# Kernel tuning notes

Hardware: AMD Instinct MI355X
Metric: run time of the kernel (lower is better)

The kernel has to match this reference:

```python
import jax, jax.numpy as jnp
import numpy as np

NLT_SIZES = (10, 19, 39, 69, 12)  # agent, action, duplex, triplet, loc
ALPHA, GAMMA, BETA = 0.25, 2.0, 1.0 / 9.0
B, A, G, T = 8, 60000, 20, 5
C = 1 + sum(NLT_SIZES)  # 150


def setup_inputs() -> dict:
    key = jax.random.key(0)
    ks = jax.random.split(key, 8)
    confidence = jax.random.normal(ks[0], (B, A, C), jnp.float32)
    predicted_locations = jax.random.normal(ks[1], (B, A, 4), jnp.float32)
    gt_locations = jax.random.normal(ks[2], (B, A, 4), jnp.float32)
    counts = jax.random.randint(ks[3], (B,), 1, G + 1, dtype=jnp.int32)
    # gt_labels: [B, G, nlts, T] with -1 tail padding per (gt, label-type) row
    labs = []
    for i, nc in enumerate(NLT_SIZES):
        l = jax.random.randint(jax.random.fold_in(ks[4], i), (B, G, T), 0, nc, dtype=jnp.int32)
        nvalid = jax.random.randint(jax.random.fold_in(ks[5], i), (B, G, 1), 1, T + 1, dtype=jnp.int32)
        l = jnp.where(jnp.arange(T, dtype=jnp.int32)[None, None, :] < nvalid, l, -1)
        labs.append(l)
    gt_labels = jnp.stack(labs, axis=2)  # [B, G, 5, T]
    # labels_bin: per-anchor match result: -1 ignore, 0 background, k in [1, counts[b]] matched gt
    pos_idx = jax.random.randint(ks[6], (B, A), 1, G + 1, dtype=jnp.int32)
    pos_idx = jnp.minimum(pos_idx, counts[:, None])
    u = jax.random.uniform(ks[7], (B, A))
    labels_bin = jnp.where(u < 0.90, 0, jnp.where(u < 0.95, -1, pos_idx)).astype(jnp.int32)
    return {
        "confidence": confidence,
        "predicted_locations": predicted_locations,
        "gt_locations": gt_locations,
        "gt_labels": gt_labels,
        "counts": counts,
        "labels_bin": labels_bin,
    }


def _head_labels(gt_labels_nlt, labels_bin, numc):
    # gt_labels_nlt: [B, G, T] int, -1 tail-padded. Vectorized one_hot_labels + gather.
    valid = (gt_labels_nlt >= 0)
    oh = jax.nn.one_hot(jnp.where(valid, gt_labels_nlt, 0), numc, dtype=jnp.float32)
    oh = oh * valid[..., None].astype(jnp.float32)
    table = (oh.sum(axis=2) > 0).astype(jnp.float32)  # [B, G, numc], multi-hot per gt
    table = jnp.pad(table, ((0, 0), (1, 0), (0, 0)))  # row 0 = background zeros -> [B, G+1, numc]
    idx = jnp.clip(labels_bin, 0, None)  # dumy_conf: ignores (-1) map to row 0
    return jnp.take_along_axis(table, idx[:, :, None], axis=1)  # [B, A, numc]


def _focal(preds, labels, mask, num_pos):
    p = jnp.clip(preds, 1e-7, 1.0 - 1e-7)
    bce = -(labels * jnp.log(p) + (1.0 - labels) * jnp.log1p(-p))
    alpha_factor = ALPHA * labels + (1.0 - ALPHA) * (1.0 - labels)
    pt = p * labels + (1.0 - p) * (1.0 - labels)
    return (bce * alpha_factor * (1.0 - pt) ** GAMMA * mask).sum() / num_pos


def reference(confidence, predicted_locations, gt_locations, gt_labels, counts, labels_bin):
    sig = jax.nn.sigmoid(confidence)
    binary_preds = sig[:, :, 0]
    heads = []
    cc = 1
    for nc in NLT_SIZES:
        heads.append(sig[:, :, cc:cc + nc])
        cc += nc

    pos = (labels_bin > 0).astype(jnp.float32)  # pos_mask
    num_pos = jnp.maximum(1.0, pos.sum())

    n = jnp.abs(predicted_locations - gt_locations)
    sl1 = jnp.where(n < BETA, 0.5 * n * n / BETA, n - 0.5 * BETA)
    regression_loss = (sl1 * pos[:, :, None]).sum() / (num_pos * 4.0)

    mask = (labels_bin > -1).astype(jnp.float32)  # exclude ignored anchors
    cls_loss = 0.0
    for i, nc in enumerate(NLT_SIZES):
        labs = _head_labels(gt_labels[:, :, i, :], labels_bin, nc)
        cls_loss = cls_loss + _focal(heads[i], labs, mask[:, :, None], num_pos)
    cls_loss = cls_loss + _focal(binary_preds, pos, mask, num_pos)  # binary head: labels_bin>0 -> 1
    return (regression_loss, cls_loss / 6.0)
```

## Files before the change

### kernel.cpp

```cpp
#include <hip/hip_runtime.h>

#define B_     8
#define A_     60000
#define C_     150
#define G_     20
#define T_     5
#define ROWS   21
#define NANCH  (B_ * A_)
#define NTOT   (B_ * A_ * C_)
#define NCHUNK (NTOT / 4)
#define TABN   (B_ * ROWS * C_)
#define BETA_  (1.0f / 9.0f)
#define NBLK   8192
#define TPB    256

__global__ void build_table(const int* __restrict__ gt_labels,
                            float* __restrict__ tab) {
    int i = blockIdx.x * blockDim.x + threadIdx.x;
    if (i >= TABN) return;
    int c  = i % C_;
    int bg = i / C_;
    int g  = bg % ROWS;
    int b  = bg / ROWS;
    float v = 0.0f;
    if (g > 0) {
        if (c == 0) {
            v = 1.0f;
        } else {
            int cc = c - 1;
            int head, k;
            if      (cc < 10)  { head = 0; k = cc; }
            else if (cc < 29)  { head = 1; k = cc - 10; }
            else if (cc < 68)  { head = 2; k = cc - 29; }
            else if (cc < 137) { head = 3; k = cc - 68; }
            else               { head = 4; k = cc - 137; }
            const int* lp = gt_labels + ((b * G_ + (g - 1)) * 5 + head) * T_;
            v = (lp[0] == k || lp[1] == k || lp[2] == k ||
                 lp[3] == k || lp[4] == k) ? 1.0f : 0.0f;
        }
    }
    tab[i] = v;
}

__device__ __forceinline__ float block_reduce_sum(float v, float* sm) {
    #pragma unroll
    for (int off = 32; off > 0; off >>= 1) v += __shfl_down(v, off, 64);
    int lane = threadIdx.x & 63, w = threadIdx.x >> 6;
    if (lane == 0) sm[w] = v;
    __syncthreads();
    float r = 0.0f;
    if (threadIdx.x == 0) r = sm[0] + sm[1] + sm[2] + sm[3];
    __syncthreads();
    return r;
}

__device__ __forceinline__ float sl1(float n) {
    return (n < BETA_) ? (0.5f / BETA_) * n * n : n - 0.5f * BETA_;
}

__device__ __forceinline__ float focal_term(float x, float L, float mf) {
    float s     = (L + L - 1.0f) * x;
    float t     = __expf(-s);
    float denom = 1.0f + t;
    float om    = t * __builtin_amdgcn_rcpf(denom);
    float ld    = __logf(denom);
    return mf * fmaf(L, -0.5f, 0.75f) * (om * om) * ld;
}

__device__ __forceinline__ float process_chunk(float4 x, int a, int c,
                                               int l0, int l1,
                                               const float* __restrict__ tab) {
    float acc = 0.0f;
    float xs[4] = {x.x, x.y, x.z, x.w};
    if (!__any((l0 | l1) != 0)) {
        #pragma unroll
        for (int j = 0; j < 4; ++j) {
            float t     = __expf(xs[j]);
            float denom = 1.0f + t;
            float om    = t * __builtin_amdgcn_rcpf(denom);
            acc += 0.75f * (om * om) * __logf(denom);
        }
    } else {
        int   b0   = a / A_;
        int   row0 = (b0 * ROWS + max(l0, 0)) * C_;
        float m0   = (l0 > -1) ? 1.0f : 0.0f;
        int   row1 = row0;
        float m1   = m0;
        if (c + 3 >= C_) {
            int b1 = (a + 1) / A_;
            row1 = (b1 * ROWS + max(l1, 0)) * C_;
            m1   = (l1 > -1) ? 1.0f : 0.0f;
        }
        #pragma unroll
        for (int j = 0; j < 4; ++j) {
            int cj = c + j;
            int rb; float mf;
            if (cj < C_) { rb = row0 + cj;       mf = m0; }
            else         { rb = row1 + cj - C_;  mf = m1; }
            acc += focal_term(xs[j], tab[rb], mf);
        }
    }
    return acc;
}

__global__ __launch_bounds__(TPB) void fused_kernel(
        const float* __restrict__ conf,
        const float* __restrict__ pred, const float* __restrict__ gtl,
        const int*   __restrict__ lb,   const float* __restrict__ tab,
        float* __restrict__ partials) {
    __shared__ float sm[4];
    float reg = 0.0f, cls = 0.0f, cnt = 0.0f;
    const int tid    = blockIdx.x * blockDim.x + threadIdx.x;
    const int stride = gridDim.x * blockDim.x;

    for (int a = tid; a < NANCH; a += stride) {
        int l = lb[a];
        if (l > 0) {
            cnt += 1.0f;
            float4 p = ((const float4*)pred)[a];
            float4 g = ((const float4*)gtl)[a];
            reg += sl1(fabsf(p.x - g.x)) + sl1(fabsf(p.y - g.y)) +
                   sl1(fabsf(p.z - g.z)) + sl1(fabsf(p.w - g.w));
        }
    }

    const float4* cp = (const float4*)conf;
    int ch = tid;
    for (; ch + stride < NCHUNK; ch += 2 * stride) {
        const int chA = ch, chB = ch + stride;
        float4 xA = cp[chA];
        float4 xB = cp[chB];
        int eA = chA * 4, aA = eA / C_, cA = eA - aA * C_;
        int eB = chB * 4, aB = eB / C_, cB = eB - aB * C_;
        int lA0 = lb[aA];
        int lA1 = (cA + 3 >= C_) ? lb[aA + 1] : lA0;
        int lB0 = lb[aB];
        int lB1 = (cB + 3 >= C_) ? lb[aB + 1] : lB0;
        cls += process_chunk(xA, aA, cA, lA0, lA1, tab);
        cls += process_chunk(xB, aB, cB, lB0, lB1, tab);
    }
    if (ch < NCHUNK) {
        float4 x = cp[ch];
        int e = ch * 4, a = e / C_, c = e - a * C_;
        int l0 = lb[a];
        int l1 = (c + 3 >= C_) ? lb[a + 1] : l0;
        cls += process_chunk(x, a, c, l0, l1, tab);
    }

    float rb = block_reduce_sum(reg, sm);
    float cb = block_reduce_sum(cls, sm);
    float nb = block_reduce_sum(cnt, sm);
    if (threadIdx.x == 0) {
        float4 w; w.x = rb; w.y = cb; w.z = nb; w.w = 0.0f;
        ((float4*)partials)[blockIdx.x] = w;
    }
}

__global__ __launch_bounds__(TPB) void finalize(
        const float* __restrict__ partials, float* __restrict__ out) {
    __shared__ float sm[4];
    float r = 0.0f, c = 0.0f, n = 0.0f;
    for (int i = threadIdx.x; i < NBLK; i += TPB) {
        float4 p = ((const float4*)partials)[i];
        r += p.x; c += p.y; n += p.z;
    }
    r = block_reduce_sum(r, sm);
    c = block_reduce_sum(c, sm);
    n = block_reduce_sum(n, sm);
    if (threadIdx.x == 0) {
        float np = fmaxf(1.0f, n);
        out[0] = r / (np * 4.0f);
        out[1] = c / (np * 6.0f);
    }
}

extern "C" void kernel_launch(void* const* d_in, const int* in_sizes, int n_in,
                              void* d_out, int out_size, void* d_ws, size_t ws_size,
                              hipStream_t stream) {
    const float* conf = (const float*)d_in[0];
    const float* pred = (const float*)d_in[1];
    const float* gt   = (const float*)d_in[2];
    const int*   gtl  = (const int*)d_in[3];
    const int*   lb   = (const int*)d_in[5];
    float* out      = (float*)d_out;
    float* partials = (float*)d_ws;
    float* tab      = (float*)d_ws + 4 * NBLK;

    build_table<<<(TABN + TPB - 1) / TPB, TPB, 0, stream>>>(gtl, tab);
    fused_kernel<<<NBLK, TPB, 0, stream>>>(conf, pred, gt, lb, tab, partials);
    finalize<<<1, TPB, 0, stream>>>(partials, out);
}
```

Baseline: 408.6 us.

## Assign wave-sized tiles of confidence chunks and use wave-uniform label loads

The confidence loop now hands each wavefront a contiguous 256-element tile instead of striding chunks per thread. Each tile spans at most three anchors, so the labels are loaded once per wave as uniform scalar loads, and the all-background fast path becomes a uniform branch rather than a ballot. The loop is unrolled by four tiles with nontemporal loads to raise memory-level parallelism and avoid polluting the cache. The finalize kernel is also widened to 1024 threads. The costs are extra index math for tiles that cross anchor or batch boundaries, and more live registers from the deeper unroll.

Measured after the change: 403.7 us. About the same (-1.2%).

```diff
diff --git a/kernel.cpp b/kernel.cpp
--- a/kernel.cpp
+++ b/kernel.cpp
@@ -9,10 +9,14 @@
 #define NANCH  (B_ * A_)
 #define NTOT   (B_ * A_ * C_)
 #define NCHUNK (NTOT / 4)
+#define NTILE  (NCHUNK / 64)
 #define TABN   (B_ * ROWS * C_)
 #define BETA_  (1.0f / 9.0f)
 #define NBLK   8192
 #define TPB    256
+#define FTPB   1024
+
+typedef float f4 __attribute__((ext_vector_type(4)));
 
 __global__ void build_table(const int* __restrict__ gt_labels,
                             float* __restrict__ tab) {
@@ -42,6 +46,7 @@
     tab[i] = v;
 }
 
+template <int NW>
 __device__ __forceinline__ float block_reduce_sum(float v, float* sm) {
     #pragma unroll
     for (int off = 32; off > 0; off >>= 1) v += __shfl_down(v, off, 64);
@@ -49,7 +54,10 @@
     if (lane == 0) sm[w] = v;
     __syncthreads();
     float r = 0.0f;
-    if (threadIdx.x == 0) r = sm[0] + sm[1] + sm[2] + sm[3];
+    if (threadIdx.x == 0) {
+        #pragma unroll
+        for (int i = 0; i < NW; ++i) r += sm[i];
+    }
     __syncthreads();
     return r;
 }
@@ -67,37 +75,45 @@
     return mf * fmaf(L, -0.5f, 0.75f) * (om * om) * ld;
 }
 
-__device__ __forceinline__ float process_chunk(float4 x, int a, int c,
-                                               int l0, int l1,
-                                               const float* __restrict__ tab) {
+__device__ __forceinline__ float tile_term(f4 x, int t, int lane,
+                                           const int* __restrict__ lb,
+                                           const float* __restrict__ tab) {
+    const int e0 = t << 8;
+    const int a0 = e0 / C_;
+    const int la0 = lb[a0];
+    const int la1 = lb[min(a0 + 1, NANCH - 1)];
+    const int la2 = lb[min(a0 + 2, NANCH - 1)];
     float acc = 0.0f;
     float xs[4] = {x.x, x.y, x.z, x.w};
-    if (!__any((l0 | l1) != 0)) {
+    if ((la0 | la1 | la2) == 0) {
         #pragma unroll
         for (int j = 0; j < 4; ++j) {
-            float t     = __expf(xs[j]);
-            float denom = 1.0f + t;
-            float om    = t * __builtin_amdgcn_rcpf(denom);
+            float u     = __expf(xs[j]);
+            float denom = 1.0f + u;
+            float om    = u * __builtin_amdgcn_rcpf(denom);
             acc += 0.75f * (om * om) * __logf(denom);
         }
     } else {
-        int   b0   = a / A_;
-        int   row0 = (b0 * ROWS + max(l0, 0)) * C_;
-        float m0   = (l0 > -1) ? 1.0f : 0.0f;
-        int   row1 = row0;
-        float m1   = m0;
-        if (c + 3 >= C_) {
-            int b1 = (a + 1) / A_;
-            row1 = (b1 * ROWS + max(l1, 0)) * C_;
-            m1   = (l1 > -1) ? 1.0f : 0.0f;
-        }
+        const int c0 = e0 - a0 * C_;
+        const int b0 = a0 / A_;
+        const int nb = (b0 + 1) * A_;
+        int off = c0 + (lane << 2);
+        int da  = (off >= C_) + (off >= 2 * C_);
+        int a   = a0 + da;
+        int cc  = off - da * C_;
+        int la  = (da == 0) ? la0 : ((da == 1) ? la1 : la2);
+        int lnx = (da == 0) ? la1 : la2;
+        int bA  = b0 + (a >= nb);
+        int bB  = b0 + (a + 1 >= nb);
+        int rowA = (bA * ROWS + max(la, 0)) * C_;
+        int rowB = (bB * ROWS + max(lnx, 0)) * C_;
+        float mA = (la  > -1) ? 1.0f : 0.0f;
+        float mB = (lnx > -1) ? 1.0f : 0.0f;
         #pragma unroll
         for (int j = 0; j < 4; ++j) {
-            int cj = c + j;
-            int rb; float mf;
-            if (cj < C_) { rb = row0 + cj;       mf = m0; }
-            else         { rb = row1 + cj - C_;  mf = m1; }
-            acc += focal_term(xs[j], tab[rb], mf);
+            int cj = cc + j;
+            if (cj < C_) acc += focal_term(xs[j], tab[rowA + cj], mA);
+            else         acc += focal_term(xs[j], tab[rowB + cj - C_], mB);
         }
     }
     return acc;
@@ -110,8 +126,8 @@
         float* __restrict__ partials) {
     __shared__ float sm[4];
     float reg = 0.0f, cls = 0.0f, cnt = 0.0f;
-    const int tid    = blockIdx.x * blockDim.x + threadIdx.x;
-    const int stride = gridDim.x * blockDim.x;
+    const int tid    = blockIdx.x * TPB + threadIdx.x;
+    const int stride = gridDim.x * TPB;
 
     for (int a = tid; a < NANCH; a += stride) {
         int l = lb[a];
@@ -124,49 +140,47 @@
         }
     }
 
-    const float4* cp = (const float4*)conf;
-    int ch = tid;
-    for (; ch + stride < NCHUNK; ch += 2 * stride) {
-        const int chA = ch, chB = ch + stride;
-        float4 xA = cp[chA];
-        float4 xB = cp[chB];
-        int eA = chA * 4, aA = eA / C_, cA = eA - aA * C_;
-        int eB = chB * 4, aB = eB / C_, cB = eB - aB * C_;
-        int lA0 = lb[aA];
-        int lA1 = (cA + 3 >= C_) ? lb[aA + 1] : lA0;
-        int lB0 = lb[aB];
-        int lB1 = (cB + 3 >= C_) ? lb[aB + 1] : lB0;
-        cls += process_chunk(xA, aA, cA, lA0, lA1, tab);
-        cls += process_chunk(xB, aB, cB, lB0, lB1, tab);
-    }
-    if (ch < NCHUNK) {
-        float4 x = cp[ch];
-        int e = ch * 4, a = e / C_, c = e - a * C_;
-        int l0 = lb[a];
-        int l1 = (c + 3 >= C_) ? lb[a + 1] : l0;
-        cls += process_chunk(x, a, c, l0, l1, tab);
-    }
-
-    float rb = block_reduce_sum(reg, sm);
-    float cb = block_reduce_sum(cls, sm);
-    float nb = block_reduce_sum(cnt, sm);
+    const f4* cp = (const f4*)conf;
+    const int lane = threadIdx.x & 63;
+    const int wv   = __builtin_amdgcn_readfirstlane(threadIdx.x >> 6);
+    const int nw   = gridDim.x * (TPB / 64);
+    int t = blockIdx.x * (TPB / 64) + wv;
+    for (; t + 3 * nw < NTILE; t += 4 * nw) {
+        const int t0 = t, t1 = t + nw, t2 = t + 2 * nw, t3 = t + 3 * nw;
+        f4 x0 = __builtin_nontemporal_load(cp + (t0 << 6) + lane);
+        f4 x1 = __builtin_nontemporal_load(cp + (t1 << 6) + lane);
+        f4 x2 = __builtin_nontemporal_load(cp + (t2 << 6) + lane);
+        f4 x3 = __builtin_nontemporal_load(cp + (t3 << 6) + lane);
+        cls += tile_term(x0, t0, lane, lb, tab);
+        cls += tile_term(x1, t1, lane, lb, tab);
+        cls += tile_term(x2, t2, lane, lb, tab);
+        cls += tile_term(x3, t3, lane, lb, tab);
+    }
+    for (; t < NTILE; t += nw) {
+        f4 x = __builtin_nontemporal_load(cp + (t << 6) + lane);
+        cls += tile_term(x, t, lane, lb, tab);
+    }
+
+    float rb = block_reduce_sum<TPB / 64>(reg, sm);
+    float cb = block_reduce_sum<TPB / 64>(cls, sm);
+    float nb = block_reduce_sum<TPB / 64>(cnt, sm);
     if (threadIdx.x == 0) {
         float4 w; w.x = rb; w.y = cb; w.z = nb; w.w = 0.0f;
         ((float4*)partials)[blockIdx.x] = w;
     }
 }
 
-__global__ __launch_bounds__(TPB) void finalize(
+__global__ __launch_bounds__(FTPB) void finalize(
         const float* __restrict__ partials, float* __restrict__ out) {
-    __shared__ float sm[4];
+    __shared__ float sm[FTPB / 64];
     float r = 0.0f, c = 0.0f, n = 0.0f;
-    for (int i = threadIdx.x; i < NBLK; i += TPB) {
+    for (int i = threadIdx.x; i < NBLK; i += FTPB) {
         float4 p = ((const float4*)partials)[i];
         r += p.x; c += p.y; n += p.z;
     }
-    r = block_reduce_sum(r, sm);
-    c = block_reduce_sum(c, sm);
-    n = block_reduce_sum(n, sm);
+    r = block_reduce_sum<FTPB / 64>(r, sm);
+    c = block_reduce_sum<FTPB / 64>(c, sm);
+    n = block_reduce_sum<FTPB / 64>(n, sm);
     if (threadIdx.x == 0) {
         float np = fmaxf(1.0f, n);
         out[0] = r / (np * 4.0f);
@@ -188,5 +202,5 @@
 
     build_table<<<(TABN + TPB - 1) / TPB, TPB, 0, stream>>>(gtl, tab);
     fused_kernel<<<NBLK, TPB, 0, stream>>>(conf, pred, gt, lb, tab, partials);
-    finalize<<<1, TPB, 0, stream>>>(partials, out);
-}
+    finalize<<<1, FTPB, 0, stream>>>(partials, out);
+}
```
